# Performance work log

Measured on AMD Instinct MI355X. Metric: run time of the kernel, lower is better.

Reference implementation:

```python
import jax, jax.numpy as jnp
import numpy as np

# Screen constants (from init_kwargs)
RES_X, RES_Y = 1024, 1024          # camera resolution (width, height)
PIX_X, PIX_Y = 1e-5, 1e-5          # pixel size in meters
BINNING = 1
NX, NY = RES_X // BINNING, RES_Y // BINNING  # effective resolution
LEFT, RIGHT = -RES_X * PIX_X / 2.0, RES_X * PIX_X / 2.0
BOTTOM, TOP = -RES_Y * PIX_Y / 2.0, RES_Y * PIX_Y / 2.0
HSTEP, VSTEP = PIX_X * BINNING, PIX_Y * BINNING
N_PARTICLES = 16_777_216
BEAM_SIGMA = 1e-3  # 1 mm rms beam size, fits in +/-5.12 mm screen extent


def setup_inputs() -> dict:
    key = jax.random.key(0)
    kx, ky = jax.random.split(key)
    xs = jax.random.normal(kx, (N_PARTICLES,), dtype=jnp.float32) * BEAM_SIGMA
    ys = jax.random.normal(ky, (N_PARTICLES,), dtype=jnp.float32) * BEAM_SIGMA
    misalignment = jnp.zeros((2,), dtype=jnp.float32)
    return {"xs": xs, "ys": ys, "misalignment": misalignment}


def reference(xs, ys, misalignment):
    # track(): subtract screen misalignment from transverse positions
    x = xs - misalignment[0]
    y = ys - misalignment[1]
    # reading(): 2D histogram over uniform pixel bin edges (torch.histogramdd)
    ix = jnp.floor((x - LEFT) / HSTEP).astype(jnp.int32)
    iy = jnp.floor((y - BOTTOM) / VSTEP).astype(jnp.int32)
    # points exactly on the rightmost/topmost edge belong to the last bin
    ix = jnp.where(x == RIGHT, NX - 1, ix)
    iy = jnp.where(y == TOP, NY - 1, iy)
    valid = (x >= LEFT) & (x <= RIGHT) & (y >= BOTTOM) & (y <= TOP)
    ix = jnp.clip(ix, 0, NX - 1)
    iy = jnp.clip(iy, 0, NY - 1)
    # image = flipud(hist.T): hist is (nx, ny) -> image[NY-1-iy, ix]
    flat = (NY - 1 - iy) * NX + ix
    w = valid.astype(jnp.float32)
    image = jnp.zeros((NY * NX,), dtype=jnp.float32).at[flat].add(w)
    return image.reshape(NY, NX)
```

## Files before the change

### kernel.cpp

```cpp
#include <hip/hip_runtime.h>
#include <hip/hip_bf16.h>


#define NXX 1024
#define NYY 1024
#define NROWS 1024
#define K3_THREADS 512
#define K3_CHUNK 16384
#define K3_G4 (K3_CHUNK / 4)
#define K3_CAP (K3_CHUNK + 1024)
#define HCOPIES 8
#define HSTRIDE 1025

static __device__ __forceinline__ unsigned int row_of(float y) {
    const float BOTTOM = (float)(-1024.0 * 1e-5 / 2.0);
    const float TOP    = (float)( 1024.0 * 1e-5 / 2.0);
    const float INVV   = 1.0f / 1e-5f;
    if (!((y >= BOTTOM) & (y <= TOP))) return 0xFFFFFFFFu;
    int iy = __float2int_rd((y - BOTTOM) * INVV);
    iy = min(max(iy, 0), NYY - 1);
    return (unsigned int)((NYY - 1) - iy);
}

static __device__ __forceinline__ unsigned int key_of32(float x, float y) {
    unsigned int r = row_of(y);
    if (r == 0xFFFFFFFFu) return 0xFFFFFFFFu;
    const float LEFT  = (float)(-1024.0 * 1e-5 / 2.0);
    const float RIGHT = (float)( 1024.0 * 1e-5 / 2.0);
    const float INVH  = 1.0f / 1e-5f;
    unsigned int col;
    if ((x >= LEFT) & (x <= RIGHT)) {
        int ix = __float2int_rd((x - LEFT) * INVH);
        col = (unsigned int)min(max(ix, 0), NXX - 1);
    } else {
        col = 0xFFFFu;
    }
    return (r << 16) | col;
}

__global__ __launch_bounds__(256) void k1_count(
    const float4* __restrict__ ys4, const float* __restrict__ mis,
    unsigned long long* __restrict__ counts64, int n4) {
    __shared__ unsigned int lc[2 * NROWS];
    const int t = threadIdx.x;
    #pragma unroll
    for (int j = 0; j < 8; ++j) lc[t + j * 256] = 0u;
    __syncthreads();
    const unsigned int cp = (t & 1) << 10;
    const float my = mis[1];
    for (int i = blockIdx.x * blockDim.x + t; i < n4; i += gridDim.x * blockDim.x) {
        float4 yv = ys4[i];
        unsigned int r;
        r = row_of(yv.x - my); if (r != 0xFFFFFFFFu) atomicAdd(&lc[cp + r], 1u);
        r = row_of(yv.y - my); if (r != 0xFFFFFFFFu) atomicAdd(&lc[cp + r], 1u);
        r = row_of(yv.z - my); if (r != 0xFFFFFFFFu) atomicAdd(&lc[cp + r], 1u);
        r = row_of(yv.w - my); if (r != 0xFFFFFFFFu) atomicAdd(&lc[cp + r], 1u);
    }
    __syncthreads();
    #pragma unroll
    for (int p = 0; p < 2; ++p) {
        unsigned int e = lc[4 * t + 2 * p] + lc[1024 + 4 * t + 2 * p];
        unsigned int o = lc[4 * t + 2 * p + 1] + lc[1024 + 4 * t + 2 * p + 1];
        if (e | o) atomicAdd(&counts64[2 * t + p],
                             (unsigned long long)e | ((unsigned long long)o << 32));
    }
}

__global__ __launch_bounds__(1024) void k2_prefix(
    const unsigned int* __restrict__ counts,
    unsigned int* __restrict__ offsets, unsigned long long* __restrict__ cursors64) {
    __shared__ unsigned int waveSums[16], waveBase[16];
    __shared__ unsigned int sB[NROWS];
    const int t = threadIdx.x, lane = t & 63, wid = t >> 6;
    unsigned int c = counts[t];
    unsigned int incl = c;
    #pragma unroll
    for (int d = 1; d < 64; d <<= 1) {
        unsigned int v = __shfl_up(incl, d, 64);
        if (lane >= d) incl += v;
    }
    if (lane == 63) waveSums[wid] = incl;
    __syncthreads();
    if (t == 0) {
        unsigned int s = 0;
        #pragma unroll
        for (int i = 0; i < 16; ++i) { waveBase[i] = s; s += waveSums[i]; }
    }
    __syncthreads();
    unsigned int excl = waveBase[wid] + incl - c;
    offsets[t] = excl;
    sB[t] = excl;
    __syncthreads();
    if (t < NROWS / 2) {
        cursors64[t] = (unsigned long long)sB[2 * t] |
                       ((unsigned long long)sB[2 * t + 1] << 32);
    }
}

__global__ __launch_bounds__(K3_THREADS) void k3_scatter(
    const float4* __restrict__ xs4, const float4* __restrict__ ys4,
    const float* __restrict__ mis, unsigned long long* __restrict__ cursors64,
    unsigned short* __restrict__ keys, unsigned int cap) {
    __shared__ unsigned int lCount[NROWS];
    __shared__ unsigned int lAdj[NROWS];
    __shared__ unsigned int waveSums[8], waveBase[8];
    __shared__ unsigned int totalKeys;
    __shared__ unsigned int reorder[K3_CAP];

    const int t = threadIdx.x, lane = t & 63, wid = t >> 6;
    lCount[t] = 0u; lCount[t + 512] = 0u;
    __syncthreads();
    const float mx = mis[0], my = mis[1];

    const int base4 = blockIdx.x * K3_G4;
    unsigned int mykey[32];
    unsigned short myrank[32];

    #pragma unroll
    for (int j = 0; j < 8; ++j) {
        int i = base4 + j * K3_THREADS + t;
        float4 xv = xs4[i], yv = ys4[i];
        #pragma unroll
        for (int e = 0; e < 4; ++e) {
            float xx = (e == 0 ? xv.x : e == 1 ? xv.y : e == 2 ? xv.z : xv.w) - mx;
            float yy = (e == 0 ? yv.x : e == 1 ? yv.y : e == 2 ? yv.z : yv.w) - my;
            unsigned int k = key_of32(xx, yy);
            mykey[j * 4 + e] = k;
            unsigned int rk = 0;
            if (k != 0xFFFFFFFFu) rk = atomicAdd(&lCount[k >> 16], 1u);
            myrank[j * 4 + e] = (unsigned short)rk;
        }
    }
    __syncthreads();

    unsigned int c0 = lCount[2 * t], c1 = lCount[2 * t + 1];
    unsigned int p0 = (cap != 0u) ? (c0 & 1u) : 0u;
    unsigned int p1 = (cap != 0u) ? (c1 & 1u) : 0u;
    unsigned int t0 = c0 + p0, t1 = c1 + p1;
    unsigned int tsum = t0 + t1;
    unsigned int incl = tsum;
    #pragma unroll
    for (int d = 1; d < 64; d <<= 1) {
        unsigned int v = __shfl_up(incl, d, 64);
        if (lane >= d) incl += v;
    }
    if (lane == 63) waveSums[wid] = incl;
    __syncthreads();
    if (t == 0) {
        unsigned int s = 0;
        #pragma unroll
        for (int i = 0; i < 8; ++i) { waveBase[i] = s; s += waveSums[i]; }
        totalKeys = s;
    }
    __syncthreads();
    unsigned int excl = waveBase[wid] + incl - tsum;
    lCount[2 * t] = excl;
    lCount[2 * t + 1] = excl + t0;
    if (tsum) {
        unsigned long long old = atomicAdd(&cursors64[t],
            (unsigned long long)t0 | ((unsigned long long)t1 << 32));
        unsigned int b0 = (unsigned int)old;
        unsigned int b1 = (unsigned int)(old >> 32);
        if (cap != 0u) {
            b0 += (unsigned int)(2 * t) * cap;
            b1 += (unsigned int)(2 * t + 1) * cap;
        }
        lAdj[2 * t]     = b0 - excl;
        lAdj[2 * t + 1] = b1 - (excl + t0);
    }
    if (p0) reorder[excl + c0]      = ((unsigned int)(2 * t) << 16) | 0xFFFFu;
    if (p1) reorder[excl + t0 + c1] = ((unsigned int)(2 * t + 1) << 16) | 0xFFFFu;
    __syncthreads();

    #pragma unroll
    for (int j = 0; j < 32; ++j) {
        unsigned int k = mykey[j];
        if (k != 0xFFFFFFFFu) {
            reorder[lCount[k >> 16] + myrank[j]] = k;
        }
    }
    __syncthreads();

    const unsigned int total = totalKeys;
    if (cap == 0) {
        for (unsigned int j = t; j < total; j += K3_THREADS) {
            unsigned int k = reorder[j];
            keys[lAdj[k >> 16] + j] = (unsigned short)k;
        }
    } else {
        const unsigned int pairs = total >> 1;
        for (unsigned int p = t; p < pairs; p += K3_THREADS) {
            uint2 kk = *(const uint2*)&reorder[2 * p];
            unsigned int row = kk.x >> 16;
            unsigned int g = lAdj[row] + 2 * p;
            unsigned int val = (kk.x & 0xFFFFu) | (kk.y << 16);
            if (g + 2 <= (row + 1) * cap)
                *(unsigned int*)&keys[g] = val;
        }
    }
}

__global__ __launch_bounds__(1024) void k4_hist(
    const unsigned short* __restrict__ keys,
    const unsigned int* __restrict__ cnts_or_deltas,
    const unsigned int* __restrict__ offsets,
    float* __restrict__ out, unsigned int cap) {
    __shared__ unsigned int hist[HCOPIES * HSTRIDE];
    const int b = blockIdx.x;
    const int r = (b & 1) ? (512 + (b >> 1)) : (511 - (b >> 1));
    for (int t = threadIdx.x; t < HCOPIES * HSTRIDE; t += 1024) hist[t] = 0u;
    __syncthreads();
    unsigned int start, cnt;
    if (cap == 0) { start = offsets[r]; cnt = cnts_or_deltas[r]; }
    else { start = (unsigned int)r * cap; cnt = cnts_or_deltas[r];
           if (cnt > cap) cnt = cap; }
    const unsigned int copy = (threadIdx.x & (HCOPIES - 1)) * HSTRIDE;
    unsigned int head = (8u - (start & 7u)) & 7u;
    if (head > cnt) head = cnt;
    if (threadIdx.x < head) {
        unsigned int c = min((unsigned int)keys[start + threadIdx.x], 1024u);
        atomicAdd(&hist[copy + c], 1u);
    }
    const unsigned int m = cnt - head;
    const uint4* pk = (const uint4*)(keys + start + head);
    const unsigned int octs = m >> 3;
    for (unsigned int q = threadIdx.x; q < octs; q += 1024) {
        uint4 v = pk[q];
        atomicAdd(&hist[copy + min(v.x & 0xFFFFu, 1024u)], 1u);
        atomicAdd(&hist[copy + min(v.x >> 16,     1024u)], 1u);
        atomicAdd(&hist[copy + min(v.y & 0xFFFFu, 1024u)], 1u);
        atomicAdd(&hist[copy + min(v.y >> 16,     1024u)], 1u);
        atomicAdd(&hist[copy + min(v.z & 0xFFFFu, 1024u)], 1u);
        atomicAdd(&hist[copy + min(v.z >> 16,     1024u)], 1u);
        atomicAdd(&hist[copy + min(v.w & 0xFFFFu, 1024u)], 1u);
        atomicAdd(&hist[copy + min(v.w >> 16,     1024u)], 1u);
    }
    const unsigned int tail = m & 7u;
    if (threadIdx.x < tail) {
        unsigned int c = min((unsigned int)keys[start + head + (octs << 3) + threadIdx.x], 1024u);
        atomicAdd(&hist[copy + c], 1u);
    }
    __syncthreads();
    float* dst = out + (size_t)r * NXX;
    for (int v = threadIdx.x; v < NXX; v += 1024) {
        unsigned int s = 0u;
        #pragma unroll
        for (int c2 = 0; c2 < HCOPIES; ++c2) s += hist[c2 * HSTRIDE + v];
        dst[v] = (float)s;
    }
}

__global__ __launch_bounds__(256) void fallback_hist(
    const float4* __restrict__ xs4, const float4* __restrict__ ys4,
    const float* __restrict__ mis, unsigned int* __restrict__ out, int n4) {
    const float mx = mis[0], my = mis[1];
    int i = blockIdx.x * blockDim.x + threadIdx.x;
    if (i >= n4) return;
    float4 xv = xs4[i], yv = ys4[i];
    #pragma unroll
    for (int e = 0; e < 4; ++e) {
        float xx = (e == 0 ? xv.x : e == 1 ? xv.y : e == 2 ? xv.z : xv.w) - mx;
        float yy = (e == 0 ? yv.x : e == 1 ? yv.y : e == 2 ? yv.z : yv.w) - my;
        unsigned int k = key_of32(xx, yy);
        if (k != 0xFFFFFFFFu && (k & 0xFFFFu) < NXX)
            atomicAdd(&out[(k >> 16) * NXX + (k & 0xFFFFu)], 1u);
    }
}
__global__ __launch_bounds__(256) void convert_kernel(unsigned int* __restrict__ buf, int n) {
    int i = blockIdx.x * blockDim.x + threadIdx.x;
    if (i < n) { unsigned int c = buf[i]; ((float*)buf)[i] = (float)c; }
}

extern "C" void kernel_launch(void* const* d_in, const int* in_sizes, int n_in,
                              void* d_out, int out_size, void* d_ws, size_t ws_size,
                              hipStream_t stream) {
    const float* xs  = (const float*)d_in[0];
    const float* ys  = (const float*)d_in[1];
    const float* mis = (const float*)d_in[2];

    const int n  = in_sizes[0];
    const int n4 = n / 4;

    unsigned char* ws = (unsigned char*)d_ws;
    unsigned long long* cursors64 = (unsigned long long*)(ws);
    unsigned int* cursors32       = (unsigned int*)(ws);
    unsigned int* counts          = (unsigned int*)(ws);
    unsigned long long* counts64  = (unsigned long long*)(ws);
    unsigned int* offsets         = (unsigned int*)(ws + 4096);
    unsigned long long* curs_ex   = (unsigned long long*)(ws + 8192);
    unsigned short* keys          = (unsigned short*)(ws + 65536);

    unsigned int cap = 0;
    if (ws_size > 65536) {
        size_t c = (ws_size - 65536) / (NROWS * sizeof(unsigned short));
        c &= ~(size_t)63;
        if (c >= 73728) cap = (unsigned int)((c > 131072) ? 131072 : c);
    }

    const int k3_grid = n / K3_CHUNK;

    if (cap) {
        hipMemsetAsync(ws, 0, 4096, stream);
        k3_scatter<<<k3_grid, K3_THREADS, 0, stream>>>(
            (const float4*)xs, (const float4*)ys, mis, cursors64, keys, cap);
        k4_hist<<<NROWS, 1024, 0, stream>>>(keys, cursors32, offsets,
                                            (float*)d_out, cap);
        return;
    }

    const size_t exact_need = 65536 + (size_t)n * sizeof(unsigned short);
    if (ws_size < exact_need) {
        unsigned int* out_u = (unsigned int*)d_out;
        hipMemsetAsync(d_out, 0, (size_t)out_size * sizeof(float), stream);
        fallback_hist<<<(n4 + 255) / 256, 256, 0, stream>>>(
            (const float4*)xs, (const float4*)ys, mis, out_u, n4);
        const int npix = NXX * NYY;
        convert_kernel<<<(npix + 255) / 256, 256, 0, stream>>>(out_u, npix);
        return;
    }

    hipMemsetAsync(ws, 0, 4096, stream);
    k1_count<<<512, 256, 0, stream>>>((const float4*)ys, mis, counts64, n4);
    k2_prefix<<<1, 1024, 0, stream>>>(counts, offsets, curs_ex);
    k3_scatter<<<k3_grid, K3_THREADS, 0, stream>>>(
        (const float4*)xs, (const float4*)ys, mis, curs_ex, keys, 0u);
    k4_hist<<<NROWS, 1024, 0, stream>>>(keys, counts, offsets, (float*)d_out, 0u);
}
```

Baseline: 188.7 us.

## Use 1024-thread scatter blocks with one row per thread and 32-bit cursors

Doubles the scatter block size to 1024 threads, so each thread handles 16 particles instead of 32 and owns a single histogram row in the per-block prefix scan. The packed 64-bit cursor atomics are replaced with plain 32-bit per-row atomics, and the prefix kernel writes cursors directly. This cuts per-thread register arrays and raises per-block parallelism, at the cost of twice as many global atomics on cursors and larger blocks that may limit occupancy given the big shared reorder buffer.

```diff
diff --git a/kernel.cpp b/kernel.cpp
--- a/kernel.cpp
+++ b/kernel.cpp
@@ -5,7 +5,7 @@
 #define NXX 1024
 #define NYY 1024
 #define NROWS 1024
-#define K3_THREADS 512
+#define K3_THREADS 1024
 #define K3_CHUNK 16384
 #define K3_G4 (K3_CHUNK / 4)
 #define K3_CAP (K3_CHUNK + 1024)
@@ -68,9 +68,8 @@
 
 __global__ __launch_bounds__(1024) void k2_prefix(
     const unsigned int* __restrict__ counts,
-    unsigned int* __restrict__ offsets, unsigned long long* __restrict__ cursors64) {
+    unsigned int* __restrict__ offsets, unsigned int* __restrict__ cursors) {
     __shared__ unsigned int waveSums[16], waveBase[16];
-    __shared__ unsigned int sB[NROWS];
     const int t = threadIdx.x, lane = t & 63, wid = t >> 6;
     unsigned int c = counts[t];
     unsigned int incl = c;
@@ -89,35 +88,30 @@
     __syncthreads();
     unsigned int excl = waveBase[wid] + incl - c;
     offsets[t] = excl;
-    sB[t] = excl;
-    __syncthreads();
-    if (t < NROWS / 2) {
-        cursors64[t] = (unsigned long long)sB[2 * t] |
-                       ((unsigned long long)sB[2 * t + 1] << 32);
-    }
-}
-
-__global__ __launch_bounds__(K3_THREADS) void k3_scatter(
+    cursors[t] = excl;
+}
+
+__global__ __launch_bounds__(K3_THREADS, 8) void k3_scatter(
     const float4* __restrict__ xs4, const float4* __restrict__ ys4,
-    const float* __restrict__ mis, unsigned long long* __restrict__ cursors64,
+    const float* __restrict__ mis, unsigned int* __restrict__ cursors,
     unsigned short* __restrict__ keys, unsigned int cap) {
     __shared__ unsigned int lCount[NROWS];
     __shared__ unsigned int lAdj[NROWS];
-    __shared__ unsigned int waveSums[8], waveBase[8];
+    __shared__ unsigned int waveSums[16], waveBase[16];
     __shared__ unsigned int totalKeys;
     __shared__ unsigned int reorder[K3_CAP];
 
     const int t = threadIdx.x, lane = t & 63, wid = t >> 6;
-    lCount[t] = 0u; lCount[t + 512] = 0u;
+    lCount[t] = 0u;
     __syncthreads();
     const float mx = mis[0], my = mis[1];
 
     const int base4 = blockIdx.x * K3_G4;
-    unsigned int mykey[32];
-    unsigned short myrank[32];
-
-    #pragma unroll
-    for (int j = 0; j < 8; ++j) {
+    unsigned int mykey[16];
+    unsigned short myrank[16];
+
+    #pragma unroll
+    for (int j = 0; j < 4; ++j) {
         int i = base4 + j * K3_THREADS + t;
         float4 xv = xs4[i], yv = ys4[i];
         #pragma unroll
@@ -133,12 +127,10 @@
     }
     __syncthreads();
 
-    unsigned int c0 = lCount[2 * t], c1 = lCount[2 * t + 1];
+    unsigned int c0 = lCount[t];
     unsigned int p0 = (cap != 0u) ? (c0 & 1u) : 0u;
-    unsigned int p1 = (cap != 0u) ? (c1 & 1u) : 0u;
-    unsigned int t0 = c0 + p0, t1 = c1 + p1;
-    unsigned int tsum = t0 + t1;
-    unsigned int incl = tsum;
+    unsigned int tt = c0 + p0;
+    unsigned int incl = tt;
     #pragma unroll
     for (int d = 1; d < 64; d <<= 1) {
         unsigned int v = __shfl_up(incl, d, 64);
@@ -149,31 +141,22 @@
     if (t == 0) {
         unsigned int s = 0;
         #pragma unroll
-        for (int i = 0; i < 8; ++i) { waveBase[i] = s; s += waveSums[i]; }
+        for (int i = 0; i < 16; ++i) { waveBase[i] = s; s += waveSums[i]; }
         totalKeys = s;
     }
     __syncthreads();
-    unsigned int excl = waveBase[wid] + incl - tsum;
-    lCount[2 * t] = excl;
-    lCount[2 * t + 1] = excl + t0;
-    if (tsum) {
-        unsigned long long old = atomicAdd(&cursors64[t],
-            (unsigned long long)t0 | ((unsigned long long)t1 << 32));
-        unsigned int b0 = (unsigned int)old;
-        unsigned int b1 = (unsigned int)(old >> 32);
-        if (cap != 0u) {
-            b0 += (unsigned int)(2 * t) * cap;
-            b1 += (unsigned int)(2 * t + 1) * cap;
-        }
-        lAdj[2 * t]     = b0 - excl;
-        lAdj[2 * t + 1] = b1 - (excl + t0);
-    }
-    if (p0) reorder[excl + c0]      = ((unsigned int)(2 * t) << 16) | 0xFFFFu;
-    if (p1) reorder[excl + t0 + c1] = ((unsigned int)(2 * t + 1) << 16) | 0xFFFFu;
-    __syncthreads();
-
-    #pragma unroll
-    for (int j = 0; j < 32; ++j) {
+    unsigned int excl = waveBase[wid] + incl - tt;
+    lCount[t] = excl;
+    if (tt) {
+        unsigned int b = atomicAdd(&cursors[t], tt);
+        if (cap != 0u) b += (unsigned int)t * cap;
+        lAdj[t] = b - excl;
+    }
+    if (p0) reorder[excl + c0] = ((unsigned int)t << 16) | 0xFFFFu;
+    __syncthreads();
+
+    #pragma unroll
+    for (int j = 0; j < 16; ++j) {
         unsigned int k = mykey[j];
         if (k != 0xFFFFFFFFu) {
             reorder[lCount[k >> 16] + myrank[j]] = k;
@@ -282,12 +265,11 @@
     const int n4 = n / 4;
 
     unsigned char* ws = (unsigned char*)d_ws;
-    unsigned long long* cursors64 = (unsigned long long*)(ws);
     unsigned int* cursors32       = (unsigned int*)(ws);
     unsigned int* counts          = (unsigned int*)(ws);
     unsigned long long* counts64  = (unsigned long long*)(ws);
     unsigned int* offsets         = (unsigned int*)(ws + 4096);
-    unsigned long long* curs_ex   = (unsigned long long*)(ws + 8192);
+    unsigned int* curs_ex         = (unsigned int*)(ws + 8192);
     unsigned short* keys          = (unsigned short*)(ws + 65536);
 
     unsigned int cap = 0;
@@ -302,7 +284,7 @@
     if (cap) {
         hipMemsetAsync(ws, 0, 4096, stream);
         k3_scatter<<<k3_grid, K3_THREADS, 0, stream>>>(
-            (const float4*)xs, (const float4*)ys, mis, cursors64, keys, cap);
+            (const float4*)xs, (const float4*)ys, mis, cursors32, keys, cap);
         k4_hist<<<NROWS, 1024, 0, stream>>>(keys, cursors32, offsets,
                                             (float*)d_out, cap);
         return;
```

New measurement: 183.9 us. 2.5% less time.
